# Kernel optimization log

Hardware: AMD Instinct MI355X
Metric: run time of the kernel (lower is better)

Reference implementation:

```python
import jax, jax.numpy as jnp
import numpy as np

N_NODES = 50000
N_EDGES = 1600000
IN_DIM = 512
HID = 128  # conv1 out = 2*HID = 256, conv2 out = HID = 128
EPS = 1e-5


def gcn_conv(x, src, dst, W, b, n_nodes):
    """PyG GCNConv: x' = D^{-1/2} (A + I) D^{-1/2} (x W) + b (self loops added)."""
    h = x @ W  # [N, out]
    loop = jnp.arange(n_nodes, dtype=src.dtype)
    s = jnp.concatenate([src, loop])  # sources incl. self loops
    d = jnp.concatenate([dst, loop])  # targets incl. self loops
    ones = jnp.ones(s.shape[0], dtype=h.dtype)
    deg = jax.ops.segment_sum(ones, d, num_segments=n_nodes)  # in-degree on targets
    dis = jnp.where(deg > 0, jax.lax.rsqrt(jnp.maximum(deg, 1.0)), 0.0)
    norm = dis[s] * dis[d]  # [E+N]
    msg = norm[:, None] * h[s]  # gather + scale, [E+N, out]
    out = jax.ops.segment_sum(msg, d, num_segments=n_nodes)  # scatter-add
    return out + b


def batch_norm(x, gamma, beta):
    """BatchNorm1d with batch statistics (biased variance), eps=1e-5."""
    mean = jnp.mean(x, axis=0)
    var = jnp.mean(jnp.square(x - mean), axis=0)
    return (x - mean) * jax.lax.rsqrt(var + EPS) * gamma + beta


def setup_inputs() -> dict:
    key = jax.random.key(0)
    ks = jax.random.split(key, 8)
    x = jax.random.normal(ks[0], (N_NODES, IN_DIM), dtype=jnp.float32)
    edge_index = jax.random.randint(ks[1], (2, N_EDGES), 0, N_NODES, dtype=jnp.int64)
    d1 = 2 * HID
    W1 = jax.random.normal(ks[2], (IN_DIM, d1), dtype=jnp.float32) / np.sqrt(IN_DIM)
    b1 = jnp.zeros((d1,), dtype=jnp.float32)
    gamma1 = jnp.ones((d1,), dtype=jnp.float32)
    beta1 = jnp.zeros((d1,), dtype=jnp.float32)
    W2 = jax.random.normal(ks[3], (d1, HID), dtype=jnp.float32) / np.sqrt(d1)
    b2 = jnp.zeros((HID,), dtype=jnp.float32)
    gamma2 = jnp.ones((HID,), dtype=jnp.float32)
    beta2 = jnp.zeros((HID,), dtype=jnp.float32)
    return {"x": x, "edge_index": edge_index, "W1": W1, "b1": b1,
            "gamma1": gamma1, "beta1": beta1, "W2": W2, "b2": b2,
            "gamma2": gamma2, "beta2": beta2}


def reference(x, edge_index, W1, b1, gamma1, beta1, W2, b2, gamma2, beta2):
    src, dst = edge_index[0], edge_index[1]
    h = gcn_conv(x, src, dst, W1, b1, N_NODES)
    h = batch_norm(h, gamma1, beta1)
    h = jax.nn.relu(h)
    # dropout: identity in eval mode (deterministic reference)
    h = gcn_conv(h, src, dst, W2, b2, N_NODES)
    h = batch_norm(h, gamma2, beta2)
    return h
```

## Files before the change

### kernel.cpp

```cpp
#include <hip/hip_runtime.h>
#include <hip/hip_bf16.h>


#define NN 50000
#define NE 1600000
#define DIN 512
#define D1 256
#define D2 128
#define EPSV 1e-5f
#define NBUCK 16
#define BSZ 3125
#define NDB 128
#define NPB 391
#define CAP 16384

typedef __attribute__((ext_vector_type(8))) short bf16x8_t;
typedef __attribute__((ext_vector_type(4))) float f32x4_t;

__device__ __forceinline__ float bf2f(unsigned short u) {
  return __uint_as_float(((unsigned int)u) << 16);
}
__device__ __forceinline__ unsigned short f2bf(float f) {
  unsigned int u = __float_as_uint(f);
  u += 0x7fffu + ((u >> 16) & 1u);
  return (unsigned short)(u >> 16);
}
__device__ __forceinline__ unsigned int pk2(float a, float b) {
  __hip_bfloat162 h = __float22bfloat162_rn(make_float2(a, b));
  union { __hip_bfloat162 h; unsigned int u; } c;
  c.h = h;
  return c.u;
}

__global__ void k_zero(int* __restrict__ gcursor, float* __restrict__ stats) {
  int i = blockIdx.x * 256 + threadIdx.x;
  if (i < NDB) gcursor[i] = 0;
  if (i < (D1 * 2 + D2 * 2)) stats[i] = 0.0f;
}

__global__ __launch_bounds__(256) void k_part(const int* __restrict__ src,
                                              const int* __restrict__ dst,
                                              int* __restrict__ gcursor,
                                              unsigned int* __restrict__ part) {
  __shared__ int hist[NDB];
  __shared__ int curs[NDB];
  const int t = threadIdx.x;
  const int EB = NE / 256;
  const int e0 = blockIdx.x * EB;
  if (t < NDB) hist[t] = 0;
  __syncthreads();
  for (int i = t; i < EB; i += 256) {
    int d = dst[e0 + i];
    atomicAdd(&hist[d / NPB], 1);
  }
  __syncthreads();
  if (t < NDB) {
    int c = hist[t];
    curs[t] = (c > 0) ? atomicAdd(&gcursor[t], c) : 0;
  }
  __syncthreads();
  for (int i = t; i < EB; i += 256) {
    int s = src[e0 + i];
    int d = dst[e0 + i];
    int b = d / NPB;
    int dl = d - b * NPB;
    int sb = (unsigned)s / BSZ;
    unsigned int w = (unsigned)s | ((unsigned)dl << 16) | ((unsigned)sb << 25);
    int pos = atomicAdd(&curs[b], 1);
    if (pos < CAP) part[(size_t)b * CAP + pos] = w;
  }
}

__global__ void k_bscan(const int* __restrict__ gcursor, int* __restrict__ ebase) {
  __shared__ int s[NDB];
  int t = threadIdx.x;
  int v = gcursor[t];
  s[t] = v;
  __syncthreads();
  for (int off = 1; off < NDB; off <<= 1) {
    int a = (t >= off) ? s[t - off] : 0;
    __syncthreads();
    s[t] += a;
    __syncthreads();
  }
  ebase[t] = s[t] - v;
  if (t == NDB - 1) ebase[NDB] = s[t];
}

__global__ __launch_bounds__(256) void k_build(const unsigned int* __restrict__ part,
                                               const int* __restrict__ gcursor,
                                               const int* __restrict__ ebase,
                                               int* __restrict__ row_ptr,
                                               float* __restrict__ dis,
                                               int* __restrict__ col) {
  const int NC = NPB * NBUCK;
  __shared__ int cnt[NC];
  __shared__ int tsum[256];
  const int b = blockIdx.x, t = threadIdx.x;
  int m = gcursor[b];
  if (m > CAP) m = CAP;
  const int base = ebase[b];
  const unsigned int* my = part + (size_t)b * CAP;
  for (int i = t; i < NC; i += 256) cnt[i] = 0;
  __syncthreads();
  for (int i = t; i < m; i += 256) {
    unsigned int w = my[i];
    atomicAdd(&cnt[((w >> 16) & 0x1ff) * NBUCK + (w >> 25)], 1);
  }
  __syncthreads();
  const int CHK = (NC + 255) / 256;
  int i0 = t * CHK;
  int sum = 0;
  for (int i = 0; i < CHK; i++) {
    int idx = i0 + i;
    if (idx < NC) sum += cnt[idx];
  }
  tsum[t] = sum;
  __syncthreads();
  for (int off = 1; off < 256; off <<= 1) {
    int a = (t >= off) ? tsum[t - off] : 0;
    __syncthreads();
    tsum[t] += a;
    __syncthreads();
  }
  int run = tsum[t] - sum;
  for (int i = 0; i < CHK; i++) {
    int idx = i0 + i;
    if (idx < NC) {
      int c = cnt[idx];
      cnt[idx] = run;
      run += c;
    }
  }
  __syncthreads();
  const int n0 = b * NPB;
  for (int dl = t; dl < NPB; dl += 256) {
    int n = n0 + dl;
    if (n < NN) {
      int st = cnt[dl * NBUCK];
      int en = (dl * NBUCK + NBUCK < NC) ? cnt[dl * NBUCK + NBUCK] : m;
      row_ptr[n] = base + st;
      dis[n] = rsqrtf((float)(en - st + 1));
    }
  }
  if (b == NDB - 1 && t == 0) row_ptr[NN] = base + m;
  __syncthreads();
  for (int i = t; i < m; i += 256) {
    unsigned int w = my[i];
    int pos = atomicAdd(&cnt[((w >> 16) & 0x1ff) * NBUCK + (w >> 25)], 1);
    col[base + pos] = w & 0xffff;
  }
}

__global__ void k_prep_w(const float* __restrict__ W1, const float* __restrict__ W2,
                         unsigned short* __restrict__ W1t, unsigned short* __restrict__ W2t) {
  int i = blockIdx.x * 256 + threadIdx.x;
  if (i < DIN * D1) {
    int n = i / DIN, k = i - n * DIN;
    W1t[i] = f2bf(W1[(size_t)k * D1 + n]);
  } else {
    int j = i - DIN * D1;
    int n = j / D1, k = j - n * D1;
    W2t[j] = f2bf(W2[(size_t)k * D2 + n]);
  }
}

__global__ __launch_bounds__(256) void k_gemm1(const float* __restrict__ A,
                                               const unsigned short* __restrict__ Bt,
                                               unsigned short* __restrict__ C, int M) {
  __shared__ unsigned short As[64 * 64];
  __shared__ unsigned short Bs[256 * 64];
  const int t = threadIdx.x;
  const int wave = t >> 6, lane = t & 63;
  const int m0 = blockIdx.x * 64;
  const int wn = wave * 64;
  const int l8 = lane >> 3;
  const int lbs = (lane & 7) ^ l8;
  const int row_c = lane & 15, quad = lane >> 4;

  f32x4_t acc[4][4];
#pragma unroll
  for (int i = 0; i < 4; i++)
#pragma unroll
    for (int j = 0; j < 4; j++) acc[i][j] = (f32x4_t){0.f, 0.f, 0.f, 0.f};

  for (int k0 = 0; k0 < DIN; k0 += 64) {
#pragma unroll
    for (int j = 0; j < 8; j++) {
      int chunk = wave * 8 + j;
      int row = chunk * 8 + l8;
      const unsigned short* g = Bt + (size_t)row * DIN + k0 + lbs * 8;
      __builtin_amdgcn_global_load_lds(
          (const __attribute__((address_space(1))) unsigned int*)g,
          (__attribute__((address_space(3))) unsigned int*)(Bs + chunk * 512), 16, 0, 0);
    }
#pragma unroll
    for (int i = 0; i < 2; i++) {
      int bid = i * 256 + t;
      int row = bid >> 3, pb = bid & 7;
      int lb = pb ^ (row & 7);
      int gm = m0 + row;
      if (gm >= M) gm = M - 1;
      const float4* s = (const float4*)(A + (size_t)gm * DIN + k0 + lb * 8);
      float4 v0 = s[0], v1 = s[1];
      uint4 o;
      o.x = pk2(v0.x, v0.y);
      o.y = pk2(v0.z, v0.w);
      o.z = pk2(v1.x, v1.y);
      o.w = pk2(v1.z, v1.w);
      *(uint4*)(As + row * 64 + pb * 8) = o;
    }
    __syncthreads();
#pragma unroll
    for (int ki = 0; ki < 2; ki++) {
      bf16x8_t af[4], bfr[4];
      int kb = ki * 4 + quad;
#pragma unroll
      for (int i = 0; i < 4; i++) {
        int ar = i * 16 + row_c;
        af[i] = *(const bf16x8_t*)(As + ar * 64 + ((kb ^ (ar & 7)) * 8));
        int br = wn + i * 16 + row_c;
        bfr[i] = *(const bf16x8_t*)(Bs + br * 64 + ((kb ^ (br & 7)) * 8));
      }
#pragma unroll
      for (int i = 0; i < 4; i++)
#pragma unroll
        for (int j = 0; j < 4; j++)
          acc[i][j] = __builtin_amdgcn_mfma_f32_16x16x32_bf16(af[i], bfr[j], acc[i][j], 0, 0, 0);
    }
    __syncthreads();
  }
#pragma unroll
  for (int i = 0; i < 4; i++) {
#pragma unroll
    for (int j = 0; j < 4; j++) {
      int colv = wn + j * 16 + row_c;
#pragma unroll
      for (int r = 0; r < 4; r++) {
        int gm = m0 + i * 16 + quad * 4 + r;
        if (gm < M) C[(size_t)gm * D1 + colv] = f2bf(acc[i][j][r]);
      }
    }
  }
}

__global__ void k_finalize1(const float* __restrict__ stats, const float* __restrict__ gamma,
                            const float* __restrict__ beta, float* __restrict__ sc1,
                            float* __restrict__ sh1) {
  int c = threadIdx.x;
  float mean = stats[c] * (1.0f / NN);
  float var = stats[D1 + c] * (1.0f / NN) - mean * mean;
  float sc = gamma[c] * rsqrtf(var + EPSV);
  sc1[c] = sc;
  sh1[c] = beta[c] - mean * sc;
}

__global__ __launch_bounds__(128) void k_gemm2(const unsigned short* __restrict__ A,
                                               const float* __restrict__ sc1,
                                               const float* __restrict__ sh1,
                                               const unsigned short* __restrict__ Bt,
                                               unsigned short* __restrict__ C, int M) {
  __shared__ unsigned short As[64 * 64];
  __shared__ unsigned short Bs[128 * 64];
  const int t = threadIdx.x;
  const int wave = t >> 6, lane = t & 63;
  const int m0 = blockIdx.x * 64;
  const int wn = wave * 64;
  const int l8 = lane >> 3;
  const int lbs = (lane & 7) ^ l8;
  const int row_c = lane & 15, quad = lane >> 4;

  f32x4_t acc[4][4];
#pragma unroll
  for (int i = 0; i < 4; i++)
#pragma unroll
    for (int j = 0; j < 4; j++) acc[i][j] = (f32x4_t){0.f, 0.f, 0.f, 0.f};

  for (int k0 = 0; k0 < D1; k0 += 64) {
#pragma unroll
    for (int j = 0; j < 8; j++) {
      int chunk = wave * 8 + j;
      int row = chunk * 8 + l8;
      const unsigned short* g = Bt + (size_t)row * D1 + k0 + lbs * 8;
      __builtin_amdgcn_global_load_lds(
          (const __attribute__((address_space(1))) unsigned int*)g,
          (__attribute__((address_space(3))) unsigned int*)(Bs + chunk * 512), 16, 0, 0);
    }
#pragma unroll
    for (int i = 0; i < 4; i++) {
      int bid = i * 128 + t;
      int row = bid >> 3, pb = bid & 7;
      int lb = pb ^ (row & 7);
      int gm = m0 + row;
      if (gm >= M) gm = M - 1;
      int colb = k0 + lb * 8;
      uint4 raw = *(const uint4*)(A + (size_t)gm * D1 + colb);
      float4 scA = *(const float4*)(sc1 + colb);
      float4 scB = *(const float4*)(sc1 + colb + 4);
      float4 shA = *(const float4*)(sh1 + colb);
      float4 shB = *(const float4*)(sh1 + colb + 4);
      float f0 = fmaxf(fmaf(bf2f((unsigned short)(raw.x & 0xffff)), scA.x, shA.x), 0.f);
      float f1 = fmaxf(fmaf(bf2f((unsigned short)(raw.x >> 16)),    scA.y, shA.y), 0.f);
      float f2 = fmaxf(fmaf(bf2f((unsigned short)(raw.y & 0xffff)), scA.z, shA.z), 0.f);
      float f3 = fmaxf(fmaf(bf2f((unsigned short)(raw.y >> 16)),    scA.w, shA.w), 0.f);
      float f4 = fmaxf(fmaf(bf2f((unsigned short)(raw.z & 0xffff)), scB.x, shB.x), 0.f);
      float f5 = fmaxf(fmaf(bf2f((unsigned short)(raw.z >> 16)),    scB.y, shB.y), 0.f);
      float f6 = fmaxf(fmaf(bf2f((unsigned short)(raw.w & 0xffff)), scB.z, shB.z), 0.f);
      float f7 = fmaxf(fmaf(bf2f((unsigned short)(raw.w >> 16)),    scB.w, shB.w), 0.f);
      uint4 o;
      o.x = pk2(f0, f1);
      o.y = pk2(f2, f3);
      o.z = pk2(f4, f5);
      o.w = pk2(f6, f7);
      *(uint4*)(As + row * 64 + pb * 8) = o;
    }
    __syncthreads();
#pragma unroll
    for (int ki = 0; ki < 2; ki++) {
      bf16x8_t af[4], bfr[4];
      int kb = ki * 4 + quad;
#pragma unroll
      for (int i = 0; i < 4; i++) {
        int ar = i * 16 + row_c;
        af[i] = *(const bf16x8_t*)(As + ar * 64 + ((kb ^ (ar & 7)) * 8));
        int br = wn + i * 16 + row_c;
        bfr[i] = *(const bf16x8_t*)(Bs + br * 64 + ((kb ^ (br & 7)) * 8));
      }
#pragma unroll
      for (int i = 0; i < 4; i++)
#pragma unroll
        for (int j = 0; j < 4; j++)
          acc[i][j] = __builtin_amdgcn_mfma_f32_16x16x32_bf16(af[i], bfr[j], acc[i][j], 0, 0, 0);
    }
    __syncthreads();
  }
#pragma unroll
  for (int i = 0; i < 4; i++) {
#pragma unroll
    for (int j = 0; j < 4; j++) {
      int colv = wn + j * 16 + row_c;
#pragma unroll
      for (int r = 0; r < 4; r++) {
        int gm = m0 + i * 16 + quad * 4 + r;
        if (gm < M) C[(size_t)gm * D2 + colv] = f2bf(acc[i][j][r]);
      }
    }
  }
}

__global__ __launch_bounds__(256) void k_agg1h(const unsigned short* __restrict__ H,
                                               const int* __restrict__ row_ptr,
                                               const int* __restrict__ col,
                                               const float* __restrict__ dis,
                                               const float* __restrict__ bias,
                                               unsigned short* __restrict__ OUT,
                                               int half) {
  int n = blockIdx.x * 4 + (threadIdx.x >> 6);
  int lane = threadIdx.x & 63;
  if (n >= NN) return;
  const unsigned short* Hh = H + half * 128;
  float dn = dis[n];
  ushort2 v = ((const ushort2*)(Hh + (size_t)n * D1))[lane];
  float wsf = dn * dn;
  float a0 = wsf * bf2f(v.x), a1 = wsf * bf2f(v.y);
  int e = row_ptr[n], e1 = row_ptr[n + 1];
  while (e < e1) {
    int cnt = e1 - e;
    if (cnt > 64) cnt = 64;
    int li = (lane < cnt) ? lane : (cnt - 1);
    int cv = col[e + li];
    float dwv = dis[cv] * dn;
    int dwu = __float_as_int(dwv);
    int b = 0;
    for (; b + 8 <= cnt; b += 8) {
      int s[8];
      float w[8];
      ushort2 u[8];
#pragma unroll
      for (int k = 0; k < 8; k++) {
        s[k] = __builtin_amdgcn_readlane(cv, b + k);
        w[k] = __int_as_float(__builtin_amdgcn_readlane(dwu, b + k));
      }
#pragma unroll
      for (int k = 0; k < 8; k++)
        u[k] = ((const ushort2*)(Hh + (size_t)s[k] * D1))[lane];
#pragma unroll
      for (int k = 0; k < 8; k++) {
        a0 += w[k] * bf2f(u[k].x);
        a1 += w[k] * bf2f(u[k].y);
      }
    }
    for (; b < cnt; b++) {
      int sK = __builtin_amdgcn_readlane(cv, b);
      float wK = __int_as_float(__builtin_amdgcn_readlane(dwu, b));
      ushort2 uK = ((const ushort2*)(Hh + (size_t)sK * D1))[lane];
      a0 += wK * bf2f(uK.x);
      a1 += wK * bf2f(uK.y);
    }
    e += cnt;
  }
  int c = half * 128 + lane * 2;
  a0 += bias[c]; a1 += bias[c + 1];
  ushort2 o;
  o.x = f2bf(a0); o.y = f2bf(a1);
  ((ushort2*)(OUT + (size_t)n * D1 + half * 128))[lane] = o;
}

__global__ __launch_bounds__(256) void k_agg2(const unsigned short* __restrict__ H,
                                              const int* __restrict__ row_ptr,
                                              const int* __restrict__ col,
                                              const float* __restrict__ dis,
                                              const float* __restrict__ bias,
                                              float* __restrict__ OUT) {
  int n = blockIdx.x * 4 + (threadIdx.x >> 6);
  int lane = threadIdx.x & 63;
  if (n >= NN) return;
  float dn = dis[n];
  ushort2 v = ((const ushort2*)(H + (size_t)n * D2))[lane];
  float wsf = dn * dn;
  float a0 = wsf * bf2f(v.x), a1 = wsf * bf2f(v.y);
  int e = row_ptr[n], e1 = row_ptr[n + 1];
  while (e < e1) {
    int cnt = e1 - e;
    if (cnt > 64) cnt = 64;
    int li = (lane < cnt) ? lane : (cnt - 1);
    int cv = col[e + li];
    float dwv = dis[cv] * dn;
    int dwu = __float_as_int(dwv);
    int b = 0;
    for (; b + 8 <= cnt; b += 8) {
      int s[8];
      float w[8];
      ushort2 u[8];
#pragma unroll
      for (int k = 0; k < 8; k++) {
        s[k] = __builtin_amdgcn_readlane(cv, b + k);
        w[k] = __int_as_float(__builtin_amdgcn_readlane(dwu, b + k));
      }
#pragma unroll
      for (int k = 0; k < 8; k++)
        u[k] = ((const ushort2*)(H + (size_t)s[k] * D2))[lane];
#pragma unroll
      for (int k = 0; k < 8; k++) {
        a0 += w[k] * bf2f(u[k].x);
        a1 += w[k] * bf2f(u[k].y);
      }
    }
    for (; b < cnt; b++) {
      int sK = __builtin_amdgcn_readlane(cv, b);
      float wK = __int_as_float(__builtin_amdgcn_readlane(dwu, b));
      ushort2 uK = ((const ushort2*)(H + (size_t)sK * D2))[lane];
      a0 += wK * bf2f(uK.x);
      a1 += wK * bf2f(uK.y);
    }
    e += cnt;
  }
  int c = lane * 2;
  a0 += bias[c]; a1 += bias[c + 1];
  ((float2*)(OUT + (size_t)n * D2))[lane] = make_float2(a0, a1);
}

__global__ void k_stats1(const unsigned short* __restrict__ X, float* __restrict__ stats) {
  int t = threadIdx.x;
  int r0 = blockIdx.x * 64;
  int r1 = (r0 + 64 < NN) ? r0 + 64 : NN;
  float s = 0.f, q = 0.f;
  for (int r = r0; r < r1; r++) {
    float v = bf2f(X[(size_t)r * D1 + t]);
    s += v;
    q += v * v;
  }
  atomicAdd(&stats[t], s);
  atomicAdd(&stats[D1 + t], q);
}

__global__ void k_stats2(const float* __restrict__ X, float* __restrict__ stats) {
  int t = threadIdx.x;
  int r0 = blockIdx.x * 128;
  int r1 = (r0 + 128 < NN) ? r0 + 128 : NN;
  float s = 0.f, q = 0.f;
  for (int r = r0; r < r1; r++) {
    float v = X[(size_t)r * D2 + t];
    s += v;
    q += v * v;
  }
  atomicAdd(&stats[t], s);
  atomicAdd(&stats[D2 + t], q);
}

__global__ void k_apply2(float* __restrict__ X, const float* __restrict__ stats,
                         const float* __restrict__ gamma, const float* __restrict__ beta) {
  int i = blockIdx.x * blockDim.x + threadIdx.x;
  int c = i & (D2 - 1);
  float mean = stats[c] * (1.0f / NN);
  float var = stats[D2 + c] * (1.0f / NN) - mean * mean;
  float sc = gamma[c] * rsqrtf(var + EPSV);
  X[i] = (X[i] - mean) * sc + beta[c];
}

extern "C" void kernel_launch(void* const* d_in, const int* in_sizes, int n_in,
                              void* d_out, int out_size, void* d_ws, size_t ws_size,
                              hipStream_t stream) {
  const float* x  = (const float*)d_in[0];
  const int* ei   = (const int*)d_in[1];
  const int* srcv = ei;
  const int* dstv = ei + NE;
  const float* W1  = (const float*)d_in[2];
  const float* b1  = (const float*)d_in[3];
  const float* g1  = (const float*)d_in[4];
  const float* be1 = (const float*)d_in[5];
  const float* W2  = (const float*)d_in[6];
  const float* b2  = (const float*)d_in[7];
  const float* g2  = (const float*)d_in[8];
  const float* be2 = (const float*)d_in[9];
  float* out = (float*)d_out;

  char* ws = (char*)d_ws;
  size_t off = 0;
  auto alloc = [&](size_t bytes) {
    size_t cur = off;
    off = (off + bytes + 255) & ~(size_t)255;
    return cur;
  };
  int* row_ptr   = (int*)(ws + alloc((NN + 1) * 4));
  float* dis     = (float*)(ws + alloc(NN * 4));
  int* gcursor   = (int*)(ws + alloc(NDB * 4));
  int* ebase     = (int*)(ws + alloc((NDB + 1) * 4));
  float* stats   = (float*)(ws + alloc((D1 * 2 + D2 * 2) * 4));
  float* sc1     = (float*)(ws + alloc(D1 * 4));
  float* sh1     = (float*)(ws + alloc(D1 * 4));
  int* col       = (int*)(ws + alloc((size_t)NE * 4));
  unsigned short* H1  = (unsigned short*)(ws + alloc((size_t)NN * D1 * 2));
  unsigned short* A1  = (unsigned short*)(ws + alloc((size_t)NN * D1 * 2));
  unsigned short* H2  = (unsigned short*)(ws + alloc((size_t)NN * D2 * 2));
  unsigned short* W1t = (unsigned short*)(ws + alloc((size_t)DIN * D1 * 2));
  unsigned short* W2t = (unsigned short*)(ws + alloc((size_t)D1 * D2 * 2));
  float* stats2 = stats + D1 * 2;
  unsigned int* part = (unsigned int*)H1;

  k_zero<<<3, 256, 0, stream>>>(gcursor, stats);
  k_part<<<256, 256, 0, stream>>>(srcv, dstv, gcursor, part);
  k_bscan<<<1, NDB, 0, stream>>>(gcursor, ebase);
  k_build<<<NDB, 256, 0, stream>>>(part, gcursor, ebase, row_ptr, dis, col);

  k_prep_w<<<(DIN * D1 + D1 * D2) / 256, 256, 0, stream>>>(W1, W2, W1t, W2t);

  const int mb = (NN + 63) / 64;

  k_gemm1<<<mb, 256, 0, stream>>>(x, W1t, H1, NN);
  k_agg1h<<<(NN + 3) / 4, 256, 0, stream>>>(H1, row_ptr, col, dis, b1, A1, 0);
  k_agg1h<<<(NN + 3) / 4, 256, 0, stream>>>(H1, row_ptr, col, dis, b1, A1, 1);
  k_stats1<<<(NN + 63) / 64, 256, 0, stream>>>(A1, stats);
  k_finalize1<<<1, 256, 0, stream>>>(stats, g1, be1, sc1, sh1);

  k_gemm2<<<mb, 128, 0, stream>>>(A1, sc1, sh1, W2t, H2, NN);
  k_agg2<<<(NN + 3) / 4, 256, 0, stream>>>(H2, row_ptr, col, dis, b2, out);
  k_stats2<<<(NN + 127) / 128, 128, 0, stream>>>(out, stats2);
  k_apply2<<<NN * D2 / 256, 256, 0, stream>>>(out, stats2, g2, be2);
}
```

Baseline: 512.7 us.

## Merge independent kernels into combined launches so graph build overlaps weight prep and GEMM1

The edge partition kernel and the weight transpose/convert now share one launch, split by block index. The CSR build and the first GEMM likewise share one launch, so the graph-building blocks run alongside the GEMM blocks instead of in separate serialized launches. The zero kernel becomes a memset, and the partition buffer gets its own workspace region instead of aliasing H1, which makes the overlap legal. This cuts launch count and idle tail time, at the cost of a shared 40KB LDS allocation that could lower GEMM occupancy.

```diff
diff --git a/kernel.cpp b/kernel.cpp
--- a/kernel.cpp
+++ b/kernel.cpp
@@ -32,42 +32,52 @@
   return c.u;
 }
 
-__global__ void k_zero(int* __restrict__ gcursor, float* __restrict__ stats) {
-  int i = blockIdx.x * 256 + threadIdx.x;
-  if (i < NDB) gcursor[i] = 0;
-  if (i < (D1 * 2 + D2 * 2)) stats[i] = 0.0f;
-}
-
-__global__ __launch_bounds__(256) void k_part(const int* __restrict__ src,
-                                              const int* __restrict__ dst,
-                                              int* __restrict__ gcursor,
-                                              unsigned int* __restrict__ part) {
+__global__ __launch_bounds__(256) void k_part_prep(const int* __restrict__ src,
+                                                   const int* __restrict__ dst,
+                                                   int* __restrict__ gcursor,
+                                                   unsigned int* __restrict__ part,
+                                                   const float* __restrict__ W1,
+                                                   const float* __restrict__ W2,
+                                                   unsigned short* __restrict__ W1t,
+                                                   unsigned short* __restrict__ W2t) {
   __shared__ int hist[NDB];
   __shared__ int curs[NDB];
   const int t = threadIdx.x;
-  const int EB = NE / 256;
-  const int e0 = blockIdx.x * EB;
-  if (t < NDB) hist[t] = 0;
-  __syncthreads();
-  for (int i = t; i < EB; i += 256) {
-    int d = dst[e0 + i];
-    atomicAdd(&hist[d / NPB], 1);
-  }
-  __syncthreads();
-  if (t < NDB) {
-    int c = hist[t];
-    curs[t] = (c > 0) ? atomicAdd(&gcursor[t], c) : 0;
-  }
-  __syncthreads();
-  for (int i = t; i < EB; i += 256) {
-    int s = src[e0 + i];
-    int d = dst[e0 + i];
-    int b = d / NPB;
-    int dl = d - b * NPB;
-    int sb = (unsigned)s / BSZ;
-    unsigned int w = (unsigned)s | ((unsigned)dl << 16) | ((unsigned)sb << 25);
-    int pos = atomicAdd(&curs[b], 1);
-    if (pos < CAP) part[(size_t)b * CAP + pos] = w;
+  if (blockIdx.x < 256) {
+    const int EB = NE / 256;
+    const int e0 = blockIdx.x * EB;
+    if (t < NDB) hist[t] = 0;
+    __syncthreads();
+    for (int i = t; i < EB; i += 256) {
+      int d = dst[e0 + i];
+      atomicAdd(&hist[d / NPB], 1);
+    }
+    __syncthreads();
+    if (t < NDB) {
+      int c = hist[t];
+      curs[t] = (c > 0) ? atomicAdd(&gcursor[t], c) : 0;
+    }
+    __syncthreads();
+    for (int i = t; i < EB; i += 256) {
+      int s = src[e0 + i];
+      int d = dst[e0 + i];
+      int b = d / NPB;
+      int dl = d - b * NPB;
+      int sb = (unsigned)s / BSZ;
+      unsigned int w = (unsigned)s | ((unsigned)dl << 16) | ((unsigned)sb << 25);
+      int pos = atomicAdd(&curs[b], 1);
+      if (pos < CAP) part[(size_t)b * CAP + pos] = w;
+    }
+  } else {
+    int i = (blockIdx.x - 256) * 256 + t;
+    if (i < DIN * D1) {
+      int n = i / DIN, k = i - n * DIN;
+      W1t[i] = f2bf(W1[(size_t)k * D1 + n]);
+    } else {
+      int j = i - DIN * D1;
+      int n = j / D1, k = j - n * D1;
+      W2t[j] = f2bf(W2[(size_t)k * D2 + n]);
+    }
   }
 }
 
@@ -87,158 +97,147 @@
   if (t == NDB - 1) ebase[NDB] = s[t];
 }
 
-__global__ __launch_bounds__(256) void k_build(const unsigned int* __restrict__ part,
-                                               const int* __restrict__ gcursor,
-                                               const int* __restrict__ ebase,
-                                               int* __restrict__ row_ptr,
-                                               float* __restrict__ dis,
-                                               int* __restrict__ col) {
-  const int NC = NPB * NBUCK;
-  __shared__ int cnt[NC];
-  __shared__ int tsum[256];
-  const int b = blockIdx.x, t = threadIdx.x;
-  int m = gcursor[b];
-  if (m > CAP) m = CAP;
-  const int base = ebase[b];
-  const unsigned int* my = part + (size_t)b * CAP;
-  for (int i = t; i < NC; i += 256) cnt[i] = 0;
-  __syncthreads();
-  for (int i = t; i < m; i += 256) {
-    unsigned int w = my[i];
-    atomicAdd(&cnt[((w >> 16) & 0x1ff) * NBUCK + (w >> 25)], 1);
-  }
-  __syncthreads();
-  const int CHK = (NC + 255) / 256;
-  int i0 = t * CHK;
-  int sum = 0;
-  for (int i = 0; i < CHK; i++) {
-    int idx = i0 + i;
-    if (idx < NC) sum += cnt[idx];
-  }
-  tsum[t] = sum;
-  __syncthreads();
-  for (int off = 1; off < 256; off <<= 1) {
-    int a = (t >= off) ? tsum[t - off] : 0;
-    __syncthreads();
-    tsum[t] += a;
-    __syncthreads();
-  }
-  int run = tsum[t] - sum;
-  for (int i = 0; i < CHK; i++) {
-    int idx = i0 + i;
-    if (idx < NC) {
-      int c = cnt[idx];
-      cnt[idx] = run;
-      run += c;
-    }
-  }
-  __syncthreads();
-  const int n0 = b * NPB;
-  for (int dl = t; dl < NPB; dl += 256) {
-    int n = n0 + dl;
-    if (n < NN) {
-      int st = cnt[dl * NBUCK];
-      int en = (dl * NBUCK + NBUCK < NC) ? cnt[dl * NBUCK + NBUCK] : m;
-      row_ptr[n] = base + st;
-      dis[n] = rsqrtf((float)(en - st + 1));
-    }
-  }
-  if (b == NDB - 1 && t == 0) row_ptr[NN] = base + m;
-  __syncthreads();
-  for (int i = t; i < m; i += 256) {
-    unsigned int w = my[i];
-    int pos = atomicAdd(&cnt[((w >> 16) & 0x1ff) * NBUCK + (w >> 25)], 1);
-    col[base + pos] = w & 0xffff;
-  }
-}
-
-__global__ void k_prep_w(const float* __restrict__ W1, const float* __restrict__ W2,
-                         unsigned short* __restrict__ W1t, unsigned short* __restrict__ W2t) {
-  int i = blockIdx.x * 256 + threadIdx.x;
-  if (i < DIN * D1) {
-    int n = i / DIN, k = i - n * DIN;
-    W1t[i] = f2bf(W1[(size_t)k * D1 + n]);
+__global__ __launch_bounds__(256) void k_build_gemm1(const unsigned int* __restrict__ part,
+                                                     const int* __restrict__ gcursor,
+                                                     const int* __restrict__ ebase,
+                                                     int* __restrict__ row_ptr,
+                                                     float* __restrict__ dis,
+                                                     int* __restrict__ col,
+                                                     const float* __restrict__ A,
+                                                     const unsigned short* __restrict__ Bt,
+                                                     unsigned short* __restrict__ C, int M) {
+  __shared__ __align__(16) char smem[40960];
+  const int t = threadIdx.x;
+  if (blockIdx.x < NDB) {
+    const int NC = NPB * NBUCK;
+    int* cnt = (int*)smem;
+    int* tsum = (int*)(smem + 25024);
+    const int b = blockIdx.x;
+    int m = gcursor[b];
+    if (m > CAP) m = CAP;
+    const int base = ebase[b];
+    const unsigned int* my = part + (size_t)b * CAP;
+    for (int i = t; i < NC; i += 256) cnt[i] = 0;
+    __syncthreads();
+    for (int i = t; i < m; i += 256) {
+      unsigned int w = my[i];
+      atomicAdd(&cnt[((w >> 16) & 0x1ff) * NBUCK + (w >> 25)], 1);
+    }
+    __syncthreads();
+    const int CHK = (NC + 255) / 256;
+    int i0 = t * CHK;
+    int sum = 0;
+    for (int i = 0; i < CHK; i++) {
+      int idx = i0 + i;
+      if (idx < NC) sum += cnt[idx];
+    }
+    tsum[t] = sum;
+    __syncthreads();
+    for (int off = 1; off < 256; off <<= 1) {
+      int a = (t >= off) ? tsum[t - off] : 0;
+      __syncthreads();
+      tsum[t] += a;
+      __syncthreads();
+    }
+    int run = tsum[t] - sum;
+    for (int i = 0; i < CHK; i++) {
+      int idx = i0 + i;
+      if (idx < NC) {
+        int c = cnt[idx];
+        cnt[idx] = run;
+        run += c;
+      }
+    }
+    __syncthreads();
+    const int n0 = b * NPB;
+    for (int dl = t; dl < NPB; dl += 256) {
+      int n = n0 + dl;
+      if (n < NN) {
+        int st = cnt[dl * NBUCK];
+        int en = (dl * NBUCK + NBUCK < NC) ? cnt[dl * NBUCK + NBUCK] : m;
+        row_ptr[n] = base + st;
+        dis[n] = rsqrtf((float)(en - st + 1));
+      }
+    }
+    if (b == NDB - 1 && t == 0) row_ptr[NN] = base + m;
+    __syncthreads();
+    for (int i = t; i < m; i += 256) {
+      unsigned int w = my[i];
+      int pos = atomicAdd(&cnt[((w >> 16) & 0x1ff) * NBUCK + (w >> 25)], 1);
+      col[base + pos] = w & 0xffff;
+    }
   } else {
-    int j = i - DIN * D1;
-    int n = j / D1, k = j - n * D1;
-    W2t[j] = f2bf(W2[(size_t)k * D2 + n]);
-  }
-}
-
-__global__ __launch_bounds__(256) void k_gemm1(const float* __restrict__ A,
-                                               const unsigned short* __restrict__ Bt,
-                                               unsigned short* __restrict__ C, int M) {
-  __shared__ unsigned short As[64 * 64];
-  __shared__ unsigned short Bs[256 * 64];
-  const int t = threadIdx.x;
-  const int wave = t >> 6, lane = t & 63;
-  const int m0 = blockIdx.x * 64;
-  const int wn = wave * 64;
-  const int l8 = lane >> 3;
-  const int lbs = (lane & 7) ^ l8;
-  const int row_c = lane & 15, quad = lane >> 4;
-
-  f32x4_t acc[4][4];
-#pragma unroll
-  for (int i = 0; i < 4; i++)
-#pragma unroll
-    for (int j = 0; j < 4; j++) acc[i][j] = (f32x4_t){0.f, 0.f, 0.f, 0.f};
-
-  for (int k0 = 0; k0 < DIN; k0 += 64) {
-#pragma unroll
-    for (int j = 0; j < 8; j++) {
-      int chunk = wave * 8 + j;
-      int row = chunk * 8 + l8;
-      const unsigned short* g = Bt + (size_t)row * DIN + k0 + lbs * 8;
-      __builtin_amdgcn_global_load_lds(
-          (const __attribute__((address_space(1))) unsigned int*)g,
-          (__attribute__((address_space(3))) unsigned int*)(Bs + chunk * 512), 16, 0, 0);
-    }
-#pragma unroll
-    for (int i = 0; i < 2; i++) {
-      int bid = i * 256 + t;
-      int row = bid >> 3, pb = bid & 7;
-      int lb = pb ^ (row & 7);
-      int gm = m0 + row;
-      if (gm >= M) gm = M - 1;
-      const float4* s = (const float4*)(A + (size_t)gm * DIN + k0 + lb * 8);
-      float4 v0 = s[0], v1 = s[1];
-      uint4 o;
-      o.x = pk2(v0.x, v0.y);
-      o.y = pk2(v0.z, v0.w);
-      o.z = pk2(v1.x, v1.y);
-      o.w = pk2(v1.z, v1.w);
-      *(uint4*)(As + row * 64 + pb * 8) = o;
-    }
-    __syncthreads();
-#pragma unroll
-    for (int ki = 0; ki < 2; ki++) {
-      bf16x8_t af[4], bfr[4];
-      int kb = ki * 4 + quad;
-#pragma unroll
-      for (int i = 0; i < 4; i++) {
-        int ar = i * 16 + row_c;
-        af[i] = *(const bf16x8_t*)(As + ar * 64 + ((kb ^ (ar & 7)) * 8));
-        int br = wn + i * 16 + row_c;
-        bfr[i] = *(const bf16x8_t*)(Bs + br * 64 + ((kb ^ (br & 7)) * 8));
-      }
-#pragma unroll
-      for (int i = 0; i < 4; i++)
-#pragma unroll
-        for (int j = 0; j < 4; j++)
-          acc[i][j] = __builtin_amdgcn_mfma_f32_16x16x32_bf16(af[i], bfr[j], acc[i][j], 0, 0, 0);
-    }
-    __syncthreads();
-  }
-#pragma unroll
-  for (int i = 0; i < 4; i++) {
-#pragma unroll
-    for (int j = 0; j < 4; j++) {
-      int colv = wn + j * 16 + row_c;
-#pragma unroll
-      for (int r = 0; r < 4; r++) {
-        int gm = m0 + i * 16 + quad * 4 + r;
-        if (gm < M) C[(size_t)gm * D1 + colv] = f2bf(acc[i][j][r]);
+    unsigned short* As = (unsigned short*)smem;
+    unsigned short* Bs = (unsigned short*)(smem + 8192);
+    const int wave = t >> 6, lane = t & 63;
+    const int m0 = (blockIdx.x - NDB) * 64;
+    const int wn = wave * 64;
+    const int l8 = lane >> 3;
+    const int lbs = (lane & 7) ^ l8;
+    const int row_c = lane & 15, quad = lane >> 4;
+
+    f32x4_t acc[4][4];
+#pragma unroll
+    for (int i = 0; i < 4; i++)
+#pragma unroll
+      for (int j = 0; j < 4; j++) acc[i][j] = (f32x4_t){0.f, 0.f, 0.f, 0.f};
+
+    for (int k0 = 0; k0 < DIN; k0 += 64) {
+#pragma unroll
+      for (int j = 0; j < 8; j++) {
+        int chunk = wave * 8 + j;
+        int row = chunk * 8 + l8;
+        const unsigned short* g = Bt + (size_t)row * DIN + k0 + lbs * 8;
+        __builtin_amdgcn_global_load_lds(
+            (const __attribute__((address_space(1))) unsigned int*)g,
+            (__attribute__((address_space(3))) unsigned int*)(Bs + chunk * 512), 16, 0, 0);
+      }
+#pragma unroll
+      for (int i = 0; i < 2; i++) {
+        int bid = i * 256 + t;
+        int row = bid >> 3, pb = bid & 7;
+        int lb = pb ^ (row & 7);
+        int gm = m0 + row;
+        if (gm >= M) gm = M - 1;
+        const float4* s = (const float4*)(A + (size_t)gm * DIN + k0 + lb * 8);
+        float4 v0 = s[0], v1 = s[1];
+        uint4 o;
+        o.x = pk2(v0.x, v0.y);
+        o.y = pk2(v0.z, v0.w);
+        o.z = pk2(v1.x, v1.y);
+        o.w = pk2(v1.z, v1.w);
+        *(uint4*)(As + row * 64 + pb * 8) = o;
+      }
+      __syncthreads();
+#pragma unroll
+      for (int ki = 0; ki < 2; ki++) {
+        bf16x8_t af[4], bfr[4];
+        int kb = ki * 4 + quad;
+#pragma unroll
+        for (int i = 0; i < 4; i++) {
+          int ar = i * 16 + row_c;
+          af[i] = *(const bf16x8_t*)(As + ar * 64 + ((kb ^ (ar & 7)) * 8));
+          int br = wn + i * 16 + row_c;
+          bfr[i] = *(const bf16x8_t*)(Bs + br * 64 + ((kb ^ (br & 7)) * 8));
+        }
+#pragma unroll
+        for (int i = 0; i < 4; i++)
+#pragma unroll
+          for (int j = 0; j < 4; j++)
+            acc[i][j] = __builtin_amdgcn_mfma_f32_16x16x32_bf16(af[i], bfr[j], acc[i][j], 0, 0, 0);
+      }
+      __syncthreads();
+    }
+#pragma unroll
+    for (int i = 0; i < 4; i++) {
+#pragma unroll
+      for (int j = 0; j < 4; j++) {
+        int colv = wn + j * 16 + row_c;
+#pragma unroll
+        for (int r = 0; r < 4; r++) {
+          int gm = m0 + i * 16 + quad * 4 + r;
+          if (gm < M) C[(size_t)gm * D1 + colv] = f2bf(acc[i][j][r]);
+        }
       }
     }
   }
@@ -522,32 +521,32 @@
     off = (off + bytes + 255) & ~(size_t)255;
     return cur;
   };
+  int* gcursor   = (int*)(ws + alloc(NDB * 4));
+  float* stats   = (float*)(ws + alloc((D1 * 2 + D2 * 2) * 4));
   int* row_ptr   = (int*)(ws + alloc((NN + 1) * 4));
   float* dis     = (float*)(ws + alloc(NN * 4));
-  int* gcursor   = (int*)(ws + alloc(NDB * 4));
   int* ebase     = (int*)(ws + alloc((NDB + 1) * 4));
-  float* stats   = (float*)(ws + alloc((D1 * 2 + D2 * 2) * 4));
   float* sc1     = (float*)(ws + alloc(D1 * 4));
   float* sh1     = (float*)(ws + alloc(D1 * 4));
   int* col       = (int*)(ws + alloc((size_t)NE * 4));
+  unsigned int* part = (unsigned int*)(ws + alloc((size_t)NDB * CAP * 4));
   unsigned short* H1  = (unsigned short*)(ws + alloc((size_t)NN * D1 * 2));
   unsigned short* A1  = (unsigned short*)(ws + alloc((size_t)NN * D1 * 2));
   unsigned short* H2  = (unsigned short*)(ws + alloc((size_t)NN * D2 * 2));
   unsigned short* W1t = (unsigned short*)(ws + alloc((size_t)DIN * D1 * 2));
   unsigned short* W2t = (unsigned short*)(ws + alloc((size_t)D1 * D2 * 2));
   float* stats2 = stats + D1 * 2;
-  unsigned int* part = (unsigned int*)H1;
-
-  k_zero<<<3, 256, 0, stream>>>(gcursor, stats);
-  k_part<<<256, 256, 0, stream>>>(srcv, dstv, gcursor, part);
+
+  hipMemsetAsync(gcursor, 0, NDB * 4 + (D1 * 2 + D2 * 2) * 4, stream);
+
+  k_part_prep<<<256 + 640, 256, 0, stream>>>(srcv, dstv, gcursor, part, W1, W2, W1t, W2t);
   k_bscan<<<1, NDB, 0, stream>>>(gcursor, ebase);
-  k_build<<<NDB, 256, 0, stream>>>(part, gcursor, ebase, row_ptr, dis, col);
-
-  k_prep_w<<<(DIN * D1 + D1 * D2) / 256, 256, 0, stream>>>(W1, W2, W1t, W2t);
 
   const int mb = (NN + 63) / 64;
 
-  k_gemm1<<<mb, 256, 0, stream>>>(x, W1t, H1, NN);
+  k_build_gemm1<<<NDB + mb, 256, 0, stream>>>(part, gcursor, ebase, row_ptr, dis, col,
+                                              x, W1t, H1, NN);
+
   k_agg1h<<<(NN + 3) / 4, 256, 0, stream>>>(H1, row_ptr, col, dis, b1, A1, 0);
   k_agg1h<<<(NN + 3) / 4, 256, 0, stream>>>(H1, row_ptr, col, dis, b1, A1, 1);
   k_stats1<<<(NN + 63) / 64, 256, 0, stream>>>(A1, stats);
```

New measurement: 494.1 us. -3.6%, faster.
